# Kernel optimization log

Hardware: AMD Instinct MI355X
Metric: run time of the kernel (lower is better)

The kernel has to match this reference:

```python
import jax, jax.numpy as jnp
import numpy as np

B, S, D, H, W1, G = 2, 4096, 768, 12, 256, 8  # W1 = one-sided window (attention_window // 2)
HD = D // H
NC = S // W1  # number of query chunks of size W1
NEG = -1e9


def setup_inputs():
    key = jax.random.key(0)
    ks = jax.random.split(key, 9)
    def w(k):
        return jax.random.normal(k, (D, D), jnp.float32) * 0.02
    zb = jnp.zeros((D,), jnp.float32)
    # mask: >0 global, 0 local, <0 masked. First G tokens are global.
    mask = jnp.zeros((B, 1, 1, S), jnp.int32).at[:, :, :, :G].set(1)
    return {
        "hidden_states": jax.random.normal(ks[0], (B, S, D), jnp.float32),
        "attention_mask": mask,
        "Wq": w(ks[1]), "bq": zb,
        "Wk": w(ks[2]), "bk": zb,
        "Wv": w(ks[3]), "bv": zb,
        "Wqg": w(ks[4]), "bqg": zb,
        "Wkg": w(ks[5]), "bkg": zb,
        "Wvg": w(ks[6]), "bvg": zb,
        "Wo": w(ks[7]), "bo": zb,
        "n_global": G,
    }


def reference(hidden_states, attention_mask, Wq, bq, Wk, bk, Wv, bv,
              Wqg, bqg, Wkg, bkg, Wvg, bvg, Wo, bo, n_global):
    g = n_global
    mask = attention_mask.reshape(B, S)
    key_neg = mask < 0  # masked-out positions
    scale = 1.0 / np.sqrt(HD)

    def heads(x):  # [B,S,D] -> [B,H,S,HD]
        return x.reshape(B, S, H, HD).transpose(0, 2, 1, 3)

    q = heads(hidden_states @ Wq + bq) * scale
    k = heads(hidden_states @ Wk + bk)
    v = heads(hidden_states @ Wv + bv)

    # ---- sliding-window (banded) scores via 3-chunk gather ----
    idx = jnp.arange(NC)[:, None] * W1 + jnp.arange(3 * W1)[None, :]  # [NC,3W] into padded seq
    k_ch = jnp.pad(k, ((0, 0), (0, 0), (W1, W1), (0, 0)))[:, :, idx]  # [B,H,NC,3W,HD]
    q_ch = q.reshape(B, H, NC, W1, HD)
    band = jnp.einsum('bhcqd,bhckd->bhcqk', q_ch, k_ch)  # [B,H,NC,W,3W]

    qi = jnp.arange(W1)
    kj = jnp.arange(3 * W1)
    band_ok = jnp.abs(kj[None, :] - W1 - qi[:, None]) <= W1        # [W,3W] |j-i|<=w
    j_abs = idx - W1                                               # absolute key index
    in_range = (j_abs >= 0) & (j_abs < S)                          # [NC,3W]
    neg_ch = jnp.pad(key_neg, ((0, 0), (W1, W1)))[:, idx]          # [B,NC,3W]
    valid = (band_ok[None, None, None]
             & in_range[None, None, :, None, :]
             & (~neg_ch)[:, None, :, None, :])                     # [B,1,NC,W,3W]
    band = jnp.where(valid, band, NEG)

    # ---- scores of every query against the global keys (regular k proj) ----
    glob = jnp.einsum('bhsd,bhgd->bhsg', q, k[:, :, :g])           # [B,H,S,G]
    glob = jnp.where(key_neg[:, None, None, :g], NEG, glob)

    scores = jnp.concatenate([glob.reshape(B, H, NC, W1, g), band], axis=-1)
    probs = jax.nn.softmax(scores, axis=-1)
    probs = jnp.where(key_neg.reshape(B, 1, NC, W1, 1), 0.0, probs)  # zero masked query rows

    v_ch = jnp.pad(v, ((0, 0), (0, 0), (W1, W1), (0, 0)))[:, :, idx]
    out = jnp.einsum('bhcqk,bhckd->bhcqd', probs[..., g:], v_ch)
    out = out + jnp.einsum('bhcqg,bhgd->bhcqd', probs[..., :g], v[:, :, :g])
    out = out.reshape(B, H, S, HD)

    # ---- global tokens: full attention with dedicated global projections ----
    qg = heads(hidden_states @ Wqg + bqg)[:, :, :g] * scale        # [B,H,G,HD]
    kg = heads(hidden_states @ Wkg + bkg)
    vg = heads(hidden_states @ Wvg + bvg)
    gs = jnp.einsum('bhgd,bhsd->bhgs', qg, kg)                     # [B,H,G,S]
    gs = jnp.where(key_neg[:, None, None, :], NEG, gs)
    gp = jax.nn.softmax(gs, axis=-1)
    og = jnp.einsum('bhgs,bhsd->bhgd', gp, vg)
    out = out.at[:, :, :g].set(og)

    merged = out.transpose(0, 2, 1, 3).reshape(B, S, D)
    return merged @ Wo + bo  # outer output projection
```

## Files before the change

### kernel.cpp

```cpp
#include <hip/hip_runtime.h>

#define BB 2
#define SS 4096
#define DD 768
#define HH 12
#define HDD 64
#define W1C 256
#define NCC 16
#define GG 8

typedef unsigned short u16;
typedef __attribute__((ext_vector_type(4))) unsigned short u16x4;
typedef __attribute__((ext_vector_type(8))) unsigned short u16x8;
typedef __attribute__((ext_vector_type(8))) short s16x8;
typedef __attribute__((ext_vector_type(4))) float f32x4;

__device__ __forceinline__ float b2f(u16 u) {
  union { unsigned int i; float f; } v;
  v.i = ((unsigned int)u) << 16;
  return v.f;
}
__device__ __forceinline__ u16 f2b(float f) {
  union { float f; unsigned int i; } v;
  v.f = f;
  unsigned int r = v.i + 0x7FFFu + ((v.i >> 16) & 1u);
  return (u16)(r >> 16);
}
__device__ __forceinline__ float fexp2(float x) {
#if __has_builtin(__builtin_amdgcn_exp2f)
  return __builtin_amdgcn_exp2f(x);
#else
  return exp2f(x);
#endif
}
__device__ __forceinline__ unsigned pk_bf16(float lo, float hi) {
  unsigned r;
  asm("v_cvt_pk_bf16_f32 %0, %1, %2" : "=v"(r) : "v"(lo), "v"(hi));
  return r;
}
__device__ __forceinline__ void load_lds16(const void* g, void* l) {
  __builtin_amdgcn_global_load_lds(
      (const __attribute__((address_space(1))) unsigned int*)g,
      (__attribute__((address_space(3))) unsigned int*)l, 16, 0, 0);
}

#define QSCALE 0.18033688011112042f

__global__ __launch_bounds__(256) void cvt_f32_bf16(
    const float* __restrict__ in, u16* __restrict__ out, int n8) {
  int i = blockIdx.x * 256 + threadIdx.x;
  if (i >= n8) return;
  const float4* p = (const float4*)(in + (size_t)i * 8);
  float4 a = p[0], b = p[1];
  u16x8 o;
  o[0] = f2b(a.x); o[1] = f2b(a.y); o[2] = f2b(a.z); o[3] = f2b(a.w);
  o[4] = f2b(b.x); o[5] = f2b(b.y); o[6] = f2b(b.z); o[7] = f2b(b.w);
  *(u16x8*)(out + (size_t)i * 8) = o;
}

struct WtArgs { const float* W[6]; };

__global__ __launch_bounds__(256) void transpose_wt(WtArgs wa,
                                                    u16* __restrict__ WT) {
  __shared__ float T[64][65];
  const int mat = blockIdx.z;
  const int k0 = blockIdx.y * 64;
  const int n0 = blockIdx.x * 64;
  const float* __restrict__ W = wa.W[mat];
  const int t = threadIdx.x;
#pragma unroll
  for (int i = 0; i < 4; i++) {
    int idx4 = t + i * 256;
    int r = idx4 >> 4, c4 = idx4 & 15;
    float4 v = *(const float4*)(W + (size_t)(k0 + r) * 768 + n0 + c4 * 4);
    T[r][c4 * 4 + 0] = v.x; T[r][c4 * 4 + 1] = v.y;
    T[r][c4 * 4 + 2] = v.z; T[r][c4 * 4 + 3] = v.w;
  }
  __syncthreads();
#pragma unroll
  for (int i = 0; i < 2; i++) {
    int ci = t + i * 256;
    int nl = ci >> 3, k8 = ci & 7;
    u16x8 o;
#pragma unroll
    for (int jj = 0; jj < 8; jj++) o[jj] = f2b(T[k8 * 8 + jj][nl]);
    *(u16x8*)(WT + ((size_t)mat * 768 + n0 + nl) * 768 + k0 + k8 * 8) = o;
  }
}

struct BiasArgs { const float* bias[5]; };

template <int MODE>
__global__ __launch_bounds__(512, 1) void gemm_bf16(
    const u16* __restrict__ A, const u16* __restrict__ WT, BiasArgs ba,
    u16* __restrict__ outb, float* __restrict__ outf) {
  constexpr int NTL = (MODE == 0) ? 15 : 3;
  constexpr int NWG = 64 * NTL;
  constexpr int NT = 12;
  constexpr int ABYTES = 128 * 64 * 2;
  constexpr int BBYTES = 256 * 64 * 2;
  constexpr int BUFB = ABYTES + BBYTES;

  extern __shared__ __align__(16) char smem[];

  const int tid = threadIdx.x;
  const int w = tid >> 6, l = tid & 63;
  const int lq = l & 15, g = l >> 4;
  const int wm = w >> 2, wn = w & 3;

  const int cpx = NWG >> 3;
  const int id = (int)blockIdx.x;
  const int swz = (id & 7) * cpx + (id >> 3);
  const int bm = swz / NTL, bn = swz % NTL;
  const int m0 = bm * 128;
  const int nw0 = bn * 256;
  const int wsel = (MODE == 0) ? (bn / 3) : 0;
  const int nmat0 = (MODE == 0) ? ((bn % 3) * 256) : (bn * 256);
  const float* __restrict__ bias = ba.bias[wsel];

  f32x4 acc[4][4];
#pragma unroll
  for (int i = 0; i < 4; i++)
#pragma unroll
    for (int j = 0; j < 4; j++) acc[i][j] = (f32x4){0.f, 0.f, 0.f, 0.f};

  auto stage = [&](int t) {
    const int k0 = t * 64;
    char* uA = smem + (t % 3) * BUFB;
    char* uB = uA + ABYTES;
#pragma unroll
    for (int j = 0; j < 2; j++) {
      const int ci = j * 8 + w;
      const int p = ci * 64 + l;
      const int row = p >> 3, sl = p & 7;
      load_lds16(A + (size_t)(m0 + row) * 768 + k0 + ((sl ^ (row & 7)) * 8),
                 uA + ci * 1024);
    }
#pragma unroll
    for (int j = 0; j < 4; j++) {
      const int ci = j * 8 + w;
      const int p = ci * 64 + l;
      const int row = p >> 3, sl = p & 7;
      load_lds16(WT + (size_t)(nw0 + row) * 768 + k0 + ((sl ^ (row & 7)) * 8),
                 uB + ci * 1024);
    }
  };

  stage(0);
  stage(1);
  asm volatile("s_waitcnt vmcnt(6)" ::: "memory");
  __builtin_amdgcn_sched_barrier(0);
  __builtin_amdgcn_s_barrier();
  __builtin_amdgcn_sched_barrier(0);

  for (int kt = 0; kt < NT; kt++) {
    const u16* rA = (const u16*)(smem + (kt % 3) * BUFB);
    const u16* rB = (const u16*)(smem + (kt % 3) * BUFB + ABYTES);

    if (kt < NT - 2) stage(kt + 2);
    __builtin_amdgcn_sched_barrier(0);

    s16x8 af[4][2], bf[4][2];
#pragma unroll
    for (int mi = 0; mi < 4; mi++) {
      const int r = wm * 64 + mi * 16 + lq;
#pragma unroll
      for (int ks = 0; ks < 2; ks++)
        af[mi][ks] =
            *(const s16x8*)(rA + r * 64 + (((ks * 4 + g) ^ (r & 7)) * 8));
    }
#pragma unroll
    for (int nj = 0; nj < 4; nj++) {
      const int r = wn * 64 + nj * 16 + lq;
#pragma unroll
      for (int ks = 0; ks < 2; ks++)
        bf[nj][ks] =
            *(const s16x8*)(rB + r * 64 + (((ks * 4 + g) ^ (r & 7)) * 8));
    }
#pragma unroll
    for (int mi = 0; mi < 4; mi++)
#pragma unroll
      for (int nj = 0; nj < 4; nj++)
#pragma unroll
        for (int ks = 0; ks < 2; ks++)
          acc[mi][nj] = __builtin_amdgcn_mfma_f32_16x16x32_bf16(
              af[mi][ks], bf[nj][ks], acc[mi][nj], 0, 0, 0);

    if (kt < NT - 2)
      asm volatile("s_waitcnt vmcnt(6)" ::: "memory");
    else
      asm volatile("s_waitcnt vmcnt(0)" ::: "memory");
    __builtin_amdgcn_sched_barrier(0);
    __builtin_amdgcn_s_barrier();
    __builtin_amdgcn_sched_barrier(0);
  }

  if (MODE == 0) {
    const float scale = (wsel == 0) ? QSCALE : 1.0f;
    u16* outw = outb + (size_t)wsel * ((size_t)BB * HH * SS * HDD);
#pragma unroll
    for (int nj = 0; nj < 4; nj++) {
      const int c = nmat0 + wn * 64 + nj * 16 + lq;
      const float bv = bias[c];
      const int h = c >> 6, hd = c & 63;
#pragma unroll
      for (int mi = 0; mi < 4; mi++) {
#pragma unroll
        for (int r = 0; r < 4; r++) {
          const int m = m0 + wm * 64 + mi * 16 + g * 4 + r;
          const int b = m >> 12, s = m & 4095;
          outw[((size_t)(b * HH + h) * SS + s) * HDD + hd] =
              f2b((acc[mi][nj][r] + bv) * scale);
        }
      }
    }
  } else {
#pragma unroll
    for (int nj = 0; nj < 4; nj++) {
      const int c = nmat0 + wn * 64 + nj * 16 + lq;
      const float bv = bias[c];
#pragma unroll
      for (int mi = 0; mi < 4; mi++) {
#pragma unroll
        for (int r = 0; r < 4; r++) {
          const int m = m0 + wm * 64 + mi * 16 + g * 4 + r;
          outf[(size_t)m * 768 + c] = acc[mi][nj][r] + bv;
        }
      }
    }
  }
}

__global__ __launch_bounds__(256) void qg_proj(
    const float* __restrict__ hs, const float* __restrict__ Wqg,
    const float* __restrict__ bqg, u16* __restrict__ QG) {
  __shared__ float hsL[8][768];
  const int bh = blockIdx.x;
  const int b = bh / HH, h = bh % HH;
  const int t = threadIdx.x;
#pragma unroll
  for (int i = 0; i < 6; i++) {
    int idx = t + i * 256;
    int row = idx / 192, c4 = idx % 192;
    *(float4*)&hsL[row][c4 * 4] =
        *(const float4*)(hs + ((size_t)b * SS + row) * DD + c4 * 4);
  }
  __syncthreads();
#pragma unroll
  for (int rep = 0; rep < 2; rep++) {
    int qi = rep * 4 + (t >> 6);
    int d = t & 63, n = h * 64 + d;
    float acc = bqg[n];
    for (int k = 0; k < DD; k++)
      acc = fmaf(hsL[qi][k], Wqg[(size_t)k * DD + n], acc);
    QG[((size_t)bh * 16 + qi) * 64 + d] = f2b(acc * QSCALE);
  }
#pragma unroll
  for (int i = 0; i < 2; i++) {
    int idx = t + i * 256;
    int row = 8 + (idx >> 6), d = idx & 63;
    QG[((size_t)bh * 16 + row) * 64 + d] = 0;
  }
}

template <int GLOBAL>
__global__ __launch_bounds__(256) void attn_mfma(
    const u16* __restrict__ Q, const u16* __restrict__ K,
    const u16* __restrict__ V, const int* __restrict__ amask,
    u16* __restrict__ ATT, float* __restrict__ Pnum,
    float* __restrict__ Pden) {
  extern __shared__ __align__(16) char smem[];
  const int tid = threadIdx.x;
  const int w = tid >> 6, lane = tid & 63;
  const int lq = lane & 15, g = lane >> 4;
  const int h = blockIdx.y, b = blockIdx.z;
  const int bh = b * HH + h;
  const size_t bhs = (size_t)bh * SS;
  const int q0 = GLOBAL ? 0 : (int)blockIdx.x * 64;
  const int split = GLOBAL ? (int)blockIdx.x : 0;

  char* Kl;
  char* VT;
  if constexpr (GLOBAL) {
    Kl = smem + w * 16384;
    VT = Kl + 8192;
  } else {
    Kl = smem;
    VT = smem + 8192;
  }

  s16x8 qf[2];
  {
    const u16* qp = GLOBAL ? (Q + ((size_t)bh * 16 + lq) * 64)
                           : (Q + (bhs + q0 + w * 16 + lq) * 64);
    qf[0] = *(const s16x8*)(qp + g * 8);
    qf[1] = *(const s16x8*)(qp + 32 + g * 8);
  }

  f32x4 oacc[4];
#pragma unroll
  for (int i = 0; i < 4; i++) oacc[i] = (f32x4){0.f, 0.f, 0.f, 0.f};
  float denom = 0.f;

  const int NT = GLOBAL ? 2 : 10;
  for (int kt = 0; kt < NT; kt++) {
    int j0, klimit;
    bool bandfree;
    if constexpr (GLOBAL) {
      j0 = split * 512 + (w * 2 + kt) * 64;
      bandfree = true;
      klimit = 64;
    } else {
      if (kt < 9) { j0 = q0 - 256 + kt * 64; bandfree = false; klimit = 64; }
      else        { j0 = 0;                  bandfree = true;  klimit = 8; }
    }

    int jm = j0 + lane;
    int mv = ((unsigned)jm < (unsigned)SS) ? amask[b * SS + jm] : -1;
    bool okk = (mv >= 0) && (lane < klimit);
    unsigned long long vm = __ballot(okk);

    if constexpr (GLOBAL) {
      asm volatile("s_waitcnt lgkmcnt(0)" ::: "memory");
      const u16* Ks = K + bhs * 64 + (size_t)j0 * 64;
#pragma unroll
      for (int i = 0; i < 8; i++) {
        int ci = i * 64 + lane;
        int row = ci >> 3, cc = ci & 7, cs = cc ^ (row & 7);
        load_lds16(Ks + row * 64 + cs * 8, Kl + i * 1024);
      }
      const u16* Vs = V + bhs * 64 + (size_t)j0 * 64;
#pragma unroll
      for (int p = 0; p < 8; p++) {
        u16x8 vv = *(const u16x8*)(Vs + (size_t)lane * 64 + p * 8);
#pragma unroll
        for (int e = 0; e < 8; e++)
          *(u16*)(VT + (p * 8 + e) * 128 + ((lane * 2) ^ (e << 4))) = vv[e];
      }
      asm volatile("s_waitcnt vmcnt(0) lgkmcnt(0)" ::: "memory");
    } else {
      __syncthreads();
      if (j0 >= 0 && j0 + 64 <= SS) {
        const u16* Ks = K + bhs * 64 + (size_t)j0 * 64;
#pragma unroll
        for (int i = 0; i < 2; i++) {
          int ci = (i * 4 + w) * 64 + lane;
          int row = ci >> 3, cc = ci & 7, cs = cc ^ (row & 7);
          load_lds16(Ks + row * 64 + cs * 8, Kl + (i * 4 + w) * 1024);
        }
      } else {
#pragma unroll
        for (int i = 0; i < 2; i++) {
          int ci = (i * 4 + w) * 64 + lane;
          int row = ci >> 3, cc = ci & 7, cs = cc ^ (row & 7);
          int jj = j0 + row;
          u16x8 val;
#pragma unroll
          for (int e = 0; e < 8; e++) val[e] = 0;
          if ((unsigned)jj < (unsigned)SS)
            val = *(const u16x8*)(K + (bhs + jj) * 64 + cs * 8);
          *(u16x8*)(Kl + ci * 16) = val;
        }
      }
#pragma unroll
      for (int p = 0; p < 2; p++) {
        int d0 = p * 32 + w * 8;
        int jj = j0 + lane;
        u16x8 vv;
#pragma unroll
        for (int e = 0; e < 8; e++) vv[e] = 0;
        if ((unsigned)jj < (unsigned)SS)
          vv = *(const u16x8*)(V + (bhs + jj) * 64 + d0);
#pragma unroll
        for (int e = 0; e < 8; e++)
          *(u16*)(VT + (d0 + e) * 128 + ((lane * 2) ^ (e << 4))) = vv[e];
      }
      asm volatile("s_waitcnt vmcnt(0)" ::: "memory");
      __syncthreads();
    }

    f32x4 sc[4];
#pragma unroll
    for (int i = 0; i < 4; i++) sc[i] = (f32x4){0.f, 0.f, 0.f, 0.f};
#pragma unroll
    for (int s = 0; s < 2; s++) {
#pragma unroll
      for (int ks = 0; ks < 4; ks++) {
        s16x8 kf = *(const s16x8*)(Kl + (ks * 16 + lq) * 128 +
                                   (((s * 4 + g) ^ (lq & 7)) << 4));
        sc[ks] = __builtin_amdgcn_mfma_f32_16x16x32_bf16(kf, qf[s], sc[ks],
                                                          0, 0, 0);
      }
    }

    {
      const unsigned mlo = (unsigned)vm, mhi = (unsigned)(vm >> 32);
      const int q_abs = q0 + w * 16 + lq;
      bool allin = bandfree;
      if constexpr (!GLOBAL) {
        const int qw = q0 + w * 16;
        allin = bandfree || (j0 >= qw - 241 && j0 <= qw + 193);
      }
      const bool fast = (vm == ~0ull) && allin;
      const int ddq = j0 + g * 4 - q_abs;
      const int gsh = g * 4;
      if (fast) {
#pragma unroll
        for (int ks = 0; ks < 4; ks++)
#pragma unroll
          for (int r = 0; r < 4; r++) {
            float p = fexp2(sc[ks][r]);
            sc[ks][r] = p;
            denom += p;
          }
      } else {
#pragma unroll
        for (int ks = 0; ks < 4; ks++)
#pragma unroll
          for (int r = 0; r < 4; r++) {
            float e = fexp2(sc[ks][r]);
            unsigned bit =
                ((ks < 2 ? mlo : mhi) >> (gsh + ((ks & 1) * 16 + r))) & 1u;
            bool ok = bit && (allin ||
                              (unsigned)(ddq + ks * 16 + r + 256) <= 512u);
            float p = ok ? e : 0.f;
            sc[ks][r] = p;
            denom += p;
          }
      }
    }

#pragma unroll
    for (int s = 0; s < 2; s++) {
      const int srcA = lq + ((g & 1) << 5);
      const bool hiSel = g >= 2;
      float L[4], H[4];
#pragma unroll
      for (int r = 0; r < 4; r++) {
        float a0 = __shfl(sc[2 * s][r], srcA);
        float a1 = __shfl(sc[2 * s + 1][r], srcA);
        L[r] = hiSel ? a1 : a0;
        float b0 = __shfl(sc[2 * s][r], srcA + 16);
        float b1 = __shfl(sc[2 * s + 1][r], srcA + 16);
        H[r] = hiSel ? b1 : b0;
      }
      union { unsigned u[4]; s16x8 v; } pf;
      pf.u[0] = pk_bf16(L[0], L[1]);
      pf.u[1] = pk_bf16(L[2], L[3]);
      pf.u[2] = pk_bf16(H[0], H[1]);
      pf.u[3] = pk_bf16(H[2], H[3]);
#pragma unroll
      for (int dblk = 0; dblk < 4; dblk++) {
        s16x8 vf = *(const s16x8*)(VT + (dblk * 16 + lq) * 128 +
                                   (((s * 4 + g) ^ (lq & 7)) << 4));
        oacc[dblk] = __builtin_amdgcn_mfma_f32_16x16x32_bf16(vf, pf.v,
                                                              oacc[dblk],
                                                              0, 0, 0);
      }
    }
  }

  denom += __shfl_xor(denom, 16);
  denom += __shfl_xor(denom, 32);
  if constexpr (!GLOBAL) {
    const int q_abs = q0 + w * 16 + lq;
    const float rowscale = (amask[b * SS + q_abs] >= 0) ? (1.f / denom) : 0.f;
    u16* orow = ATT + ((size_t)b * SS + q_abs) * DD + h * 64;
#pragma unroll
    for (int dblk = 0; dblk < 4; dblk++) {
      u16x4 o;
#pragma unroll
      for (int r = 0; r < 4; r++) o[r] = f2b(oacc[dblk][r] * rowscale);
      *(u16x4*)(orow + dblk * 16 + g * 4) = o;
    }
  } else {
    const int pidx = split * 4 + w;
    float* np = Pnum + ((size_t)bh * 32 + pidx) * 1024;
#pragma unroll
    for (int dblk = 0; dblk < 4; dblk++)
#pragma unroll
      for (int r = 0; r < 4; r++)
        np[(dblk * 16 + g * 4 + r) * 16 + lq] = oacc[dblk][r];
    Pden[((size_t)bh * 32 + pidx) * 16 + lq] = denom;
  }
}

__global__ __launch_bounds__(512) void gmerge(const float* __restrict__ Pnum,
                                              const float* __restrict__ Pden,
                                              u16* __restrict__ ATT) {
  const int bh = blockIdx.x;
  const int b = bh / HH, h = bh % HH;
  const int t = threadIdx.x;
  const int q = t >> 6, d = t & 63;
  float num = 0.f, den = 0.f;
#pragma unroll 4
  for (int p = 0; p < 32; p++) {
    num += Pnum[((size_t)bh * 32 + p) * 1024 + d * 16 + q];
    den += Pden[((size_t)bh * 32 + p) * 16 + q];
  }
  ATT[((size_t)b * SS + q) * DD + h * 64 + d] = f2b(num / den);
}

extern "C" void kernel_launch(void* const* d_in, const int* in_sizes, int n_in,
                              void* d_out, int out_size, void* d_ws,
                              size_t ws_size, hipStream_t stream) {
  const float* hs = (const float*)d_in[0];
  const int* amask = (const int*)d_in[1];
  const float* Wq = (const float*)d_in[2];
  const float* bq = (const float*)d_in[3];
  const float* Wk = (const float*)d_in[4];
  const float* bk = (const float*)d_in[5];
  const float* Wv = (const float*)d_in[6];
  const float* bv = (const float*)d_in[7];
  const float* Wqg = (const float*)d_in[8];
  const float* bqg = (const float*)d_in[9];
  const float* Wkg = (const float*)d_in[10];
  const float* bkg = (const float*)d_in[11];
  const float* Wvg = (const float*)d_in[12];
  const float* bvg = (const float*)d_in[13];
  const float* Wo = (const float*)d_in[14];
  const float* bo = (const float*)d_in[15];
  float* out = (float*)d_out;

  char* ws = (char*)d_ws;
  const size_t QSZB = (size_t)BB * HH * SS * HDD * 2;
  u16* Qb = (u16*)(ws + 0);
  u16* Kb = (u16*)(ws + QSZB);
  u16* Vb = (u16*)(ws + 2 * QSZB);
  u16* KGb = (u16*)(ws + 3 * QSZB);
  u16* VGb = (u16*)(ws + 4 * QSZB);
  u16* Ab = (u16*)(ws + 5 * QSZB);
  u16* WTb = (u16*)(ws + 6 * QSZB);
  u16* ATTb = (u16*)(ws + 6 * QSZB + 7077888);
  u16* QGb = (u16*)(ws + 7 * QSZB + 7077888);
  float* Pnum = (float*)(ws + 7 * QSZB + 7077888 + 49152);
  float* Pden = (float*)(ws + 7 * QSZB + 7077888 + 49152 + 3145728);

  hipLaunchKernelGGL(cvt_f32_bf16, dim3(3072), dim3(256), 0, stream, hs, Ab,
                     (int)((size_t)BB * SS * DD / 8));

  WtArgs wa;
  wa.W[0] = Wq; wa.W[1] = Wk; wa.W[2] = Wv;
  wa.W[3] = Wkg; wa.W[4] = Wvg; wa.W[5] = Wo;
  hipLaunchKernelGGL(transpose_wt, dim3(12, 12, 6), dim3(256), 0, stream, wa,
                     WTb);

  BiasArgs b0;
  b0.bias[0] = bq; b0.bias[1] = bk; b0.bias[2] = bv;
  b0.bias[3] = bkg; b0.bias[4] = bvg;
  hipLaunchKernelGGL((gemm_bf16<0>), dim3(960), dim3(512), 147456, stream,
                     Ab, WTb, b0, Qb, (float*)nullptr);

  hipLaunchKernelGGL(qg_proj, dim3(24), dim3(256), 0, stream, hs, Wqg, bqg,
                     QGb);

  hipLaunchKernelGGL((attn_mfma<1>), dim3(8, HH, BB), dim3(256), 65536,
                     stream, QGb, KGb, VGb, amask, (u16*)nullptr, Pnum, Pden);

  hipLaunchKernelGGL((attn_mfma<0>), dim3(64, HH, BB), dim3(256), 16384,
                     stream, Qb, Kb, Vb, amask, ATTb, (float*)nullptr,
                     (float*)nullptr);

  hipLaunchKernelGGL(gmerge, dim3(24), dim3(512), 0, stream, Pnum, Pden, ATTb);

  BiasArgs b1;
  for (int i = 0; i < 5; i++) b1.bias[i] = bo;
  hipLaunchKernelGGL((gemm_bf16<1>), dim3(192), dim3(512), 147456, stream,
                     ATTb, WTb + (size_t)5 * 768 * 768, b1, (u16*)nullptr,
                     out);
}
```

Before: 203.1 us.

## Fuse prep kernels and double-buffer K/V tiles in band attention

The bf16 conversion, weight transpose and global-query projection are merged into one launch, removing two kernel launches. The band attention becomes its own kernel with 512-thread blocks covering 128 queries and double-buffered LDS. The next K tile is loaded asynchronously and the next V tile is held in registers while the current tile is computed. This is meant to hide global-load latency and cut the number of blocks. The cost is more LDS per block, an extra barrier per iteration, and register pressure from holding V in registers.

```diff
diff --git a/kernel.cpp b/kernel.cpp
--- a/kernel.cpp
+++ b/kernel.cpp
@@ -46,45 +46,77 @@
 
 #define QSCALE 0.18033688011112042f
 
-__global__ __launch_bounds__(256) void cvt_f32_bf16(
-    const float* __restrict__ in, u16* __restrict__ out, int n8) {
-  int i = blockIdx.x * 256 + threadIdx.x;
-  if (i >= n8) return;
-  const float4* p = (const float4*)(in + (size_t)i * 8);
-  float4 a = p[0], b = p[1];
-  u16x8 o;
-  o[0] = f2b(a.x); o[1] = f2b(a.y); o[2] = f2b(a.z); o[3] = f2b(a.w);
-  o[4] = f2b(b.x); o[5] = f2b(b.y); o[6] = f2b(b.z); o[7] = f2b(b.w);
-  *(u16x8*)(out + (size_t)i * 8) = o;
-}
-
 struct WtArgs { const float* W[6]; };
 
-__global__ __launch_bounds__(256) void transpose_wt(WtArgs wa,
-                                                    u16* __restrict__ WT) {
-  __shared__ float T[64][65];
-  const int mat = blockIdx.z;
-  const int k0 = blockIdx.y * 64;
-  const int n0 = blockIdx.x * 64;
-  const float* __restrict__ W = wa.W[mat];
+__global__ __launch_bounds__(256) void prep(
+    const float* __restrict__ hs, WtArgs wa, const float* __restrict__ Wqg,
+    const float* __restrict__ bqg, u16* __restrict__ Ab,
+    u16* __restrict__ WT, u16* __restrict__ QG) {
+  __shared__ __align__(16) char pshm[24576];
+  const int bid = blockIdx.x;
   const int t = threadIdx.x;
-#pragma unroll
-  for (int i = 0; i < 4; i++) {
-    int idx4 = t + i * 256;
-    int r = idx4 >> 4, c4 = idx4 & 15;
-    float4 v = *(const float4*)(W + (size_t)(k0 + r) * 768 + n0 + c4 * 4);
-    T[r][c4 * 4 + 0] = v.x; T[r][c4 * 4 + 1] = v.y;
-    T[r][c4 * 4 + 2] = v.z; T[r][c4 * 4 + 3] = v.w;
-  }
-  __syncthreads();
-#pragma unroll
-  for (int i = 0; i < 2; i++) {
-    int ci = t + i * 256;
-    int nl = ci >> 3, k8 = ci & 7;
+
+  if (bid < 3072) {
+    int i = bid * 256 + t;
+    const float4* p = (const float4*)(hs + (size_t)i * 8);
+    float4 a = p[0], b = p[1];
     u16x8 o;
-#pragma unroll
-    for (int jj = 0; jj < 8; jj++) o[jj] = f2b(T[k8 * 8 + jj][nl]);
-    *(u16x8*)(WT + ((size_t)mat * 768 + n0 + nl) * 768 + k0 + k8 * 8) = o;
+    o[0] = f2b(a.x); o[1] = f2b(a.y); o[2] = f2b(a.z); o[3] = f2b(a.w);
+    o[4] = f2b(b.x); o[5] = f2b(b.y); o[6] = f2b(b.z); o[7] = f2b(b.w);
+    *(u16x8*)(Ab + (size_t)i * 8) = o;
+  } else if (bid < 3936) {
+    float (*T)[65] = (float (*)[65])pshm;
+    const int t2 = bid - 3072;
+    const int mat = t2 / 144;
+    const int rem = t2 % 144;
+    const int k0 = (rem / 12) * 64;
+    const int n0 = (rem % 12) * 64;
+    const float* __restrict__ W = wa.W[mat];
+#pragma unroll
+    for (int i = 0; i < 4; i++) {
+      int idx4 = t + i * 256;
+      int r = idx4 >> 4, c4 = idx4 & 15;
+      float4 v = *(const float4*)(W + (size_t)(k0 + r) * 768 + n0 + c4 * 4);
+      T[r][c4 * 4 + 0] = v.x; T[r][c4 * 4 + 1] = v.y;
+      T[r][c4 * 4 + 2] = v.z; T[r][c4 * 4 + 3] = v.w;
+    }
+    __syncthreads();
+#pragma unroll
+    for (int i = 0; i < 2; i++) {
+      int ci = t + i * 256;
+      int nl = ci >> 3, k8 = ci & 7;
+      u16x8 o;
+#pragma unroll
+      for (int jj = 0; jj < 8; jj++) o[jj] = f2b(T[k8 * 8 + jj][nl]);
+      *(u16x8*)(WT + ((size_t)mat * 768 + n0 + nl) * 768 + k0 + k8 * 8) = o;
+    }
+  } else {
+    float (*hsL)[768] = (float (*)[768])pshm;
+    const int bh = bid - 3936;
+    const int b = bh / HH, h = bh % HH;
+#pragma unroll
+    for (int i = 0; i < 6; i++) {
+      int idx = t + i * 256;
+      int row = idx / 192, c4 = idx % 192;
+      *(float4*)&hsL[row][c4 * 4] =
+          *(const float4*)(hs + ((size_t)b * SS + row) * DD + c4 * 4);
+    }
+    __syncthreads();
+#pragma unroll
+    for (int rep = 0; rep < 2; rep++) {
+      int qi = rep * 4 + (t >> 6);
+      int d = t & 63, n = h * 64 + d;
+      float acc = bqg[n];
+      for (int k = 0; k < DD; k++)
+        acc = fmaf(hsL[qi][k], Wqg[(size_t)k * DD + n], acc);
+      QG[((size_t)bh * 16 + qi) * 64 + d] = f2b(acc * QSCALE);
+    }
+#pragma unroll
+    for (int i = 0; i < 2; i++) {
+      int idx = t + i * 256;
+      int row = 8 + (idx >> 6), d = idx & 63;
+      QG[((size_t)bh * 16 + row) * 64 + d] = 0;
+    }
   }
 }
 
@@ -231,68 +263,22 @@
   }
 }
 
-__global__ __launch_bounds__(256) void qg_proj(
-    const float* __restrict__ hs, const float* __restrict__ Wqg,
-    const float* __restrict__ bqg, u16* __restrict__ QG) {
-  __shared__ float hsL[8][768];
-  const int bh = blockIdx.x;
-  const int b = bh / HH, h = bh % HH;
-  const int t = threadIdx.x;
-#pragma unroll
-  for (int i = 0; i < 6; i++) {
-    int idx = t + i * 256;
-    int row = idx / 192, c4 = idx % 192;
-    *(float4*)&hsL[row][c4 * 4] =
-        *(const float4*)(hs + ((size_t)b * SS + row) * DD + c4 * 4);
-  }
-  __syncthreads();
-#pragma unroll
-  for (int rep = 0; rep < 2; rep++) {
-    int qi = rep * 4 + (t >> 6);
-    int d = t & 63, n = h * 64 + d;
-    float acc = bqg[n];
-    for (int k = 0; k < DD; k++)
-      acc = fmaf(hsL[qi][k], Wqg[(size_t)k * DD + n], acc);
-    QG[((size_t)bh * 16 + qi) * 64 + d] = f2b(acc * QSCALE);
-  }
-#pragma unroll
-  for (int i = 0; i < 2; i++) {
-    int idx = t + i * 256;
-    int row = 8 + (idx >> 6), d = idx & 63;
-    QG[((size_t)bh * 16 + row) * 64 + d] = 0;
-  }
-}
-
-template <int GLOBAL>
-__global__ __launch_bounds__(256) void attn_mfma(
+__global__ __launch_bounds__(512, 4) void attn_band(
     const u16* __restrict__ Q, const u16* __restrict__ K,
     const u16* __restrict__ V, const int* __restrict__ amask,
-    u16* __restrict__ ATT, float* __restrict__ Pnum,
-    float* __restrict__ Pden) {
-  extern __shared__ __align__(16) char smem[];
+    u16* __restrict__ ATT) {
+  __shared__ __align__(16) char smem[32768];
   const int tid = threadIdx.x;
   const int w = tid >> 6, lane = tid & 63;
   const int lq = lane & 15, g = lane >> 4;
   const int h = blockIdx.y, b = blockIdx.z;
   const int bh = b * HH + h;
   const size_t bhs = (size_t)bh * SS;
-  const int q0 = GLOBAL ? 0 : (int)blockIdx.x * 64;
-  const int split = GLOBAL ? (int)blockIdx.x : 0;
-
-  char* Kl;
-  char* VT;
-  if constexpr (GLOBAL) {
-    Kl = smem + w * 16384;
-    VT = Kl + 8192;
-  } else {
-    Kl = smem;
-    VT = smem + 8192;
-  }
+  const int q0 = (int)blockIdx.x * 128;
 
   s16x8 qf[2];
   {
-    const u16* qp = GLOBAL ? (Q + ((size_t)bh * 16 + lq) * 64)
-                           : (Q + (bhs + q0 + w * 16 + lq) * 64);
+    const u16* qp = Q + (bhs + q0 + w * 16 + lq) * 64;
     qf[0] = *(const s16x8*)(qp + g * 8);
     qf[1] = *(const s16x8*)(qp + 32 + g * 8);
   }
@@ -302,82 +288,61 @@
   for (int i = 0; i < 4; i++) oacc[i] = (f32x4){0.f, 0.f, 0.f, 0.f};
   float denom = 0.f;
 
-  const int NT = GLOBAL ? 2 : 10;
+  const int NT = 11;
+  u16x8 vreg;
+
+  auto jof = [&](int t) { return t < 10 ? q0 - 256 + t * 64 : 0; };
+
+  auto stage_issue = [&](int t) {
+    const int j0 = jof(t);
+    char* Kb_ = smem + (t & 1) * 16384;
+    const int row = tid >> 3, sl = tid & 7;
+    if (j0 >= 0 && j0 + 64 <= SS) {
+      load_lds16(K + (bhs + j0 + row) * 64 + ((sl ^ (row & 7)) * 8),
+                 Kb_ + w * 1024);
+    } else {
+      int jj = j0 + row;
+      u16x8 val;
+#pragma unroll
+      for (int e = 0; e < 8; e++) val[e] = 0;
+      if ((unsigned)jj < (unsigned)SS)
+        val = *(const u16x8*)(K + (bhs + jj) * 64 + ((sl ^ (row & 7)) * 8));
+      *(u16x8*)(Kb_ + tid * 16) = val;
+    }
+    int jj = j0 + lane;
+    u16x8 vv;
+#pragma unroll
+    for (int e = 0; e < 8; e++) vv[e] = 0;
+    if ((unsigned)jj < (unsigned)SS)
+      vv = *(const u16x8*)(V + (bhs + jj) * 64 + w * 8);
+    vreg = vv;
+  };
+
+  stage_issue(0);
+
   for (int kt = 0; kt < NT; kt++) {
-    int j0, klimit;
-    bool bandfree;
-    if constexpr (GLOBAL) {
-      j0 = split * 512 + (w * 2 + kt) * 64;
-      bandfree = true;
-      klimit = 64;
-    } else {
-      if (kt < 9) { j0 = q0 - 256 + kt * 64; bandfree = false; klimit = 64; }
-      else        { j0 = 0;                  bandfree = true;  klimit = 8; }
-    }
+    const int j0 = jof(kt);
+    const int cur = kt & 1;
+    char* Kl = smem + cur * 16384;
+    char* VT = Kl + 8192;
+    const bool bandfree = (kt == 10);
+    const int klimit = bandfree ? 8 : 64;
 
     int jm = j0 + lane;
     int mv = ((unsigned)jm < (unsigned)SS) ? amask[b * SS + jm] : -1;
     bool okk = (mv >= 0) && (lane < klimit);
     unsigned long long vm = __ballot(okk);
 
-    if constexpr (GLOBAL) {
-      asm volatile("s_waitcnt lgkmcnt(0)" ::: "memory");
-      const u16* Ks = K + bhs * 64 + (size_t)j0 * 64;
-#pragma unroll
-      for (int i = 0; i < 8; i++) {
-        int ci = i * 64 + lane;
-        int row = ci >> 3, cc = ci & 7, cs = cc ^ (row & 7);
-        load_lds16(Ks + row * 64 + cs * 8, Kl + i * 1024);
-      }
-      const u16* Vs = V + bhs * 64 + (size_t)j0 * 64;
-#pragma unroll
-      for (int p = 0; p < 8; p++) {
-        u16x8 vv = *(const u16x8*)(Vs + (size_t)lane * 64 + p * 8);
-#pragma unroll
-        for (int e = 0; e < 8; e++)
-          *(u16*)(VT + (p * 8 + e) * 128 + ((lane * 2) ^ (e << 4))) = vv[e];
-      }
-      asm volatile("s_waitcnt vmcnt(0) lgkmcnt(0)" ::: "memory");
-    } else {
-      __syncthreads();
-      if (j0 >= 0 && j0 + 64 <= SS) {
-        const u16* Ks = K + bhs * 64 + (size_t)j0 * 64;
-#pragma unroll
-        for (int i = 0; i < 2; i++) {
-          int ci = (i * 4 + w) * 64 + lane;
-          int row = ci >> 3, cc = ci & 7, cs = cc ^ (row & 7);
-          load_lds16(Ks + row * 64 + cs * 8, Kl + (i * 4 + w) * 1024);
-        }
-      } else {
-#pragma unroll
-        for (int i = 0; i < 2; i++) {
-          int ci = (i * 4 + w) * 64 + lane;
-          int row = ci >> 3, cc = ci & 7, cs = cc ^ (row & 7);
-          int jj = j0 + row;
-          u16x8 val;
-#pragma unroll
-          for (int e = 0; e < 8; e++) val[e] = 0;
-          if ((unsigned)jj < (unsigned)SS)
-            val = *(const u16x8*)(K + (bhs + jj) * 64 + cs * 8);
-          *(u16x8*)(Kl + ci * 16) = val;
-        }
-      }
-#pragma unroll
-      for (int p = 0; p < 2; p++) {
-        int d0 = p * 32 + w * 8;
-        int jj = j0 + lane;
-        u16x8 vv;
-#pragma unroll
-        for (int e = 0; e < 8; e++) vv[e] = 0;
-        if ((unsigned)jj < (unsigned)SS)
-          vv = *(const u16x8*)(V + (bhs + jj) * 64 + d0);
-#pragma unroll
-        for (int e = 0; e < 8; e++)
-          *(u16*)(VT + (d0 + e) * 128 + ((lane * 2) ^ (e << 4))) = vv[e];
-      }
-      asm volatile("s_waitcnt vmcnt(0)" ::: "memory");
-      __syncthreads();
-    }
+    asm volatile("s_waitcnt vmcnt(0)" ::: "memory");
+#pragma unroll
+    for (int e = 0; e < 8; e++)
+      *(u16*)(VT + (w * 8 + e) * 128 + ((lane * 2) ^ (e << 4))) = vreg[e];
+    asm volatile("s_waitcnt lgkmcnt(0)" ::: "memory");
+    __builtin_amdgcn_sched_barrier(0);
+    __builtin_amdgcn_s_barrier();
+    __builtin_amdgcn_sched_barrier(0);
+
+    if (kt + 1 < NT) stage_issue(kt + 1);
 
     f32x4 sc[4];
 #pragma unroll
@@ -396,11 +361,8 @@
     {
       const unsigned mlo = (unsigned)vm, mhi = (unsigned)(vm >> 32);
       const int q_abs = q0 + w * 16 + lq;
-      bool allin = bandfree;
-      if constexpr (!GLOBAL) {
-        const int qw = q0 + w * 16;
-        allin = bandfree || (j0 >= qw - 241 && j0 <= qw + 193);
-      }
+      const int qw = q0 + w * 16;
+      const bool allin = bandfree || (j0 >= qw - 241 && j0 <= qw + 193);
       const bool fast = (vm == ~0ull) && allin;
       const int ddq = j0 + g * 4 - q_abs;
       const int gsh = g * 4;
@@ -458,31 +420,161 @@
                                                               0, 0, 0);
       }
     }
+
+    __builtin_amdgcn_sched_barrier(0);
+    __builtin_amdgcn_s_barrier();
+    __builtin_amdgcn_sched_barrier(0);
   }
 
   denom += __shfl_xor(denom, 16);
   denom += __shfl_xor(denom, 32);
-  if constexpr (!GLOBAL) {
-    const int q_abs = q0 + w * 16 + lq;
-    const float rowscale = (amask[b * SS + q_abs] >= 0) ? (1.f / denom) : 0.f;
-    u16* orow = ATT + ((size_t)b * SS + q_abs) * DD + h * 64;
-#pragma unroll
-    for (int dblk = 0; dblk < 4; dblk++) {
-      u16x4 o;
-#pragma unroll
-      for (int r = 0; r < 4; r++) o[r] = f2b(oacc[dblk][r] * rowscale);
-      *(u16x4*)(orow + dblk * 16 + g * 4) = o;
-    }
-  } else {
-    const int pidx = split * 4 + w;
-    float* np = Pnum + ((size_t)bh * 32 + pidx) * 1024;
-#pragma unroll
-    for (int dblk = 0; dblk < 4; dblk++)
-#pragma unroll
-      for (int r = 0; r < 4; r++)
-        np[(dblk * 16 + g * 4 + r) * 16 + lq] = oacc[dblk][r];
-    Pden[((size_t)bh * 32 + pidx) * 16 + lq] = denom;
-  }
+  const int q_abs = q0 + w * 16 + lq;
+  const float rowscale = (amask[b * SS + q_abs] >= 0) ? (1.f / denom) : 0.f;
+  u16* orow = ATT + ((size_t)b * SS + q_abs) * DD + h * 64;
+#pragma unroll
+  for (int dblk = 0; dblk < 4; dblk++) {
+    u16x4 o;
+#pragma unroll
+    for (int r = 0; r < 4; r++) o[r] = f2b(oacc[dblk][r] * rowscale);
+    *(u16x4*)(orow + dblk * 16 + g * 4) = o;
+  }
+}
+
+__global__ __launch_bounds__(256) void attn_global(
+    const u16* __restrict__ Q, const u16* __restrict__ K,
+    const u16* __restrict__ V, const int* __restrict__ amask,
+    float* __restrict__ Pnum, float* __restrict__ Pden) {
+  extern __shared__ __align__(16) char smem[];
+  const int tid = threadIdx.x;
+  const int w = tid >> 6, lane = tid & 63;
+  const int lq = lane & 15, g = lane >> 4;
+  const int h = blockIdx.y, b = blockIdx.z;
+  const int bh = b * HH + h;
+  const size_t bhs = (size_t)bh * SS;
+  const int split = (int)blockIdx.x;
+
+  char* Kl = smem + w * 16384;
+  char* VT = Kl + 8192;
+
+  s16x8 qf[2];
+  {
+    const u16* qp = Q + ((size_t)bh * 16 + lq) * 64;
+    qf[0] = *(const s16x8*)(qp + g * 8);
+    qf[1] = *(const s16x8*)(qp + 32 + g * 8);
+  }
+
+  f32x4 oacc[4];
+#pragma unroll
+  for (int i = 0; i < 4; i++) oacc[i] = (f32x4){0.f, 0.f, 0.f, 0.f};
+  float denom = 0.f;
+
+  for (int kt = 0; kt < 2; kt++) {
+    const int j0 = split * 512 + (w * 2 + kt) * 64;
+
+    int jm = j0 + lane;
+    int mv = amask[b * SS + jm];
+    unsigned long long vm = __ballot(mv >= 0);
+
+    asm volatile("s_waitcnt lgkmcnt(0)" ::: "memory");
+    const u16* Ks = K + bhs * 64 + (size_t)j0 * 64;
+#pragma unroll
+    for (int i = 0; i < 8; i++) {
+      int ci = i * 64 + lane;
+      int row = ci >> 3, cc = ci & 7, cs = cc ^ (row & 7);
+      load_lds16(Ks + row * 64 + cs * 8, Kl + i * 1024);
+    }
+    const u16* Vs = V + bhs * 64 + (size_t)j0 * 64;
+#pragma unroll
+    for (int p = 0; p < 8; p++) {
+      u16x8 vv = *(const u16x8*)(Vs + (size_t)lane * 64 + p * 8);
+#pragma unroll
+      for (int e = 0; e < 8; e++)
+        *(u16*)(VT + (p * 8 + e) * 128 + ((lane * 2) ^ (e << 4))) = vv[e];
+    }
+    asm volatile("s_waitcnt vmcnt(0) lgkmcnt(0)" ::: "memory");
+
+    f32x4 sc[4];
+#pragma unroll
+    for (int i = 0; i < 4; i++) sc[i] = (f32x4){0.f, 0.f, 0.f, 0.f};
+#pragma unroll
+    for (int s = 0; s < 2; s++) {
+#pragma unroll
+      for (int ks = 0; ks < 4; ks++) {
+        s16x8 kf = *(const s16x8*)(Kl + (ks * 16 + lq) * 128 +
+                                   (((s * 4 + g) ^ (lq & 7)) << 4));
+        sc[ks] = __builtin_amdgcn_mfma_f32_16x16x32_bf16(kf, qf[s], sc[ks],
+                                                          0, 0, 0);
+      }
+    }
+
+    {
+      const unsigned mlo = (unsigned)vm, mhi = (unsigned)(vm >> 32);
+      const bool fast = (vm == ~0ull);
+      const int gsh = g * 4;
+      if (fast) {
+#pragma unroll
+        for (int ks = 0; ks < 4; ks++)
+#pragma unroll
+          for (int r = 0; r < 4; r++) {
+            float p = fexp2(sc[ks][r]);
+            sc[ks][r] = p;
+            denom += p;
+          }
+      } else {
+#pragma unroll
+        for (int ks = 0; ks < 4; ks++)
+#pragma unroll
+          for (int r = 0; r < 4; r++) {
+            float e = fexp2(sc[ks][r]);
+            unsigned bit =
+                ((ks < 2 ? mlo : mhi) >> (gsh + ((ks & 1) * 16 + r))) & 1u;
+            float p = bit ? e : 0.f;
+            sc[ks][r] = p;
+            denom += p;
+          }
+      }
+    }
+
+#pragma unroll
+    for (int s = 0; s < 2; s++) {
+      const int srcA = lq + ((g & 1) << 5);
+      const bool hiSel = g >= 2;
+      float L[4], H[4];
+#pragma unroll
+      for (int r = 0; r < 4; r++) {
+        float a0 = __shfl(sc[2 * s][r], srcA);
+        float a1 = __shfl(sc[2 * s + 1][r], srcA);
+        L[r] = hiSel ? a1 : a0;
+        float b0 = __shfl(sc[2 * s][r], srcA + 16);
+        float b1 = __shfl(sc[2 * s + 1][r], srcA + 16);
+        H[r] = hiSel ? b1 : b0;
+      }
+      union { unsigned u[4]; s16x8 v; } pf;
+      pf.u[0] = pk_bf16(L[0], L[1]);
+      pf.u[1] = pk_bf16(L[2], L[3]);
+      pf.u[2] = pk_bf16(H[0], H[1]);
+      pf.u[3] = pk_bf16(H[2], H[3]);
+#pragma unroll
+      for (int dblk = 0; dblk < 4; dblk++) {
+        s16x8 vf = *(const s16x8*)(VT + (dblk * 16 + lq) * 128 +
+                                   (((s * 4 + g) ^ (lq & 7)) << 4));
+        oacc[dblk] = __builtin_amdgcn_mfma_f32_16x16x32_bf16(vf, pf.v,
+                                                              oacc[dblk],
+                                                              0, 0, 0);
+      }
+    }
+  }
+
+  denom += __shfl_xor(denom, 16);
+  denom += __shfl_xor(denom, 32);
+  const int pidx = split * 4 + w;
+  float* np = Pnum + ((size_t)bh * 32 + pidx) * 1024;
+#pragma unroll
+  for (int dblk = 0; dblk < 4; dblk++)
+#pragma unroll
+    for (int r = 0; r < 4; r++)
+      np[(dblk * 16 + g * 4 + r) * 16 + lq] = oacc[dblk][r];
+  Pden[((size_t)bh * 32 + pidx) * 16 + lq] = denom;
 }
 
 __global__ __launch_bounds__(512) void gmerge(const float* __restrict__ Pnum,
@@ -536,14 +628,11 @@
   float* Pnum = (float*)(ws + 7 * QSZB + 7077888 + 49152);
   float* Pden = (float*)(ws + 7 * QSZB + 7077888 + 49152 + 3145728);
 
-  hipLaunchKernelGGL(cvt_f32_bf16, dim3(3072), dim3(256), 0, stream, hs, Ab,
-                     (int)((size_t)BB * SS * DD / 8));
-
   WtArgs wa;
   wa.W[0] = Wq; wa.W[1] = Wk; wa.W[2] = Wv;
   wa.W[3] = Wkg; wa.W[4] = Wvg; wa.W[5] = Wo;
-  hipLaunchKernelGGL(transpose_wt, dim3(12, 12, 6), dim3(256), 0, stream, wa,
-                     WTb);
+  hipLaunchKernelGGL(prep, dim3(3960), dim3(256), 0, stream, hs, wa, Wqg,
+                     bqg, Ab, WTb, QGb);
 
   BiasArgs b0;
   b0.bias[0] = bq; b0.bias[1] = bk; b0.bias[2] = bv;
@@ -551,15 +640,11 @@
   hipLaunchKernelGGL((gemm_bf16<0>), dim3(960), dim3(512), 147456, stream,
                      Ab, WTb, b0, Qb, (float*)nullptr);
 
-  hipLaunchKernelGGL(qg_proj, dim3(24), dim3(256), 0, stream, hs, Wqg, bqg,
-                     QGb);
-
-  hipLaunchKernelGGL((attn_mfma<1>), dim3(8, HH, BB), dim3(256), 65536,
-                     stream, QGb, KGb, VGb, amask, (u16*)nullptr, Pnum, Pden);
-
-  hipLaunchKernelGGL((attn_mfma<0>), dim3(64, HH, BB), dim3(256), 16384,
-                     stream, Qb, Kb, Vb, amask, ATTb, (float*)nullptr,
-                     (float*)nullptr);
+  hipLaunchKernelGGL(attn_global, dim3(8, HH, BB), dim3(256), 65536, stream,
+                     QGb, KGb, VGb, amask, Pnum, Pden);
+
+  hipLaunchKernelGGL(attn_band, dim3(32, HH, BB), dim3(512), 0, stream, Qb,
+                     Kb, Vb, amask, ATTb);
 
   hipLaunchKernelGGL(gmerge, dim3(24), dim3(512), 0, stream, Pnum, Pden, ATTb);
 
```

Result: faster. 198.1 us (-2.5%).
